# Performance work log

Measured on AMD Instinct MI355X. Metric: run time of the kernel, lower is better.

The kernel has to match this reference:

```python
import jax, jax.numpy as jnp
import numpy as np

# Config mirroring init kwargs (bias_base_type='full', no bos/eos, n_channels=1)
SHAPE_ = 64          # side of the 2D grid; seq_len = SHAPE_**2
N_CHANNELS = 1
N_HEADS = 16
EMB_DIM = 64
BATCH = 8
SEQ_LEN = SHAPE_ * SHAPE_ * N_CHANNELS
N = 2 * SHAPE_ - 1   # linear-convolution length


def setup_inputs() -> dict:
    key = jax.random.key(0)
    k1, k2 = jax.random.split(key)
    v = jax.random.normal(k1, (BATCH, SEQ_LEN, N_HEADS, EMB_DIM), dtype=jnp.float32)
    w = jax.random.normal(k2, (1, N_HEADS, N), dtype=jnp.float32)
    return {"v": v, "w": w}


def reference(v, w):
    shape_ = SHAPE_
    n = 2 * shape_ - 1
    B, S, H, E = v.shape
    C = N_CHANNELS

    # _compute_z_fft with bias_base_type='full', seq_len=shape_:
    # z = w[..., shape_-seq_len : shape_+seq_len-1] == w[..., 0:n]
    z_fft = jnp.fft.rfft(w[..., :n])                       # (1, H, n//2+1)

    # [B,S,H,E] -> [B,E,H,S] -> [B,E,H,s1,s2,C] -> [B,E,C,s1,H,s2]
    v_ = jnp.transpose(v, (0, 3, 2, 1)).reshape(B, E, H, shape_, shape_, C)
    v_ = jnp.transpose(v_, (0, 1, 5, 3, 2, 4))

    pad = ((0, 0),) * 4 + ((shape_ - 1, 0),)
    # sum over s1 (axis -3) -> function of s2; left-pad and rfft
    v_m_fft = jnp.fft.rfft(jnp.pad(v_.sum(-3), pad))       # [B,E,C,H,nr]
    # swap s1/s2, sum over s2 -> function of s1
    u_m_fft = jnp.fft.rfft(jnp.pad(jnp.transpose(v_, (0, 1, 2, 5, 4, 3)).sum(-3), pad))

    zf = jnp.expand_dims(z_fft, axis=1)                    # (1, 1, H, nr) broadcasts
    RxV = jnp.fft.irfft(v_m_fft * zf, n=n)[..., :shape_]   # [B,E,C,H,shape_]
    RxU = jnp.fft.irfft(u_m_fft * zf, n=n)[..., :shape_]   # [B,E,C,H,shape_]

    # outer sum over (s1, s2) grid
    pbv = RxV[..., None, :] + RxU[..., None]               # [B,E,C,H,s1,s2]
    pbv = pbv.reshape(B, E, C, H, shape_ * shape_)
    pbv = jnp.transpose(pbv, (0, 1, 3, 4, 2)).reshape(B, E, H, S)
    return jnp.transpose(pbv, (0, 3, 2, 1))                # [B, S, H, E]
```

## Files before the change

kernel.cpp:

```cpp
#include <hip/hip_runtime.h>


typedef float f4 __attribute__((ext_vector_type(4)));

__global__ __launch_bounds__(256, 4) void k1_reduce(
    const f4* __restrict__ v4,
    f4* __restrict__ vm_part,
    f4* __restrict__ um_ws)
{
    __shared__ f4 um_w[4][16][8];

    const int bid   = blockIdx.x;
    const int hcb   = bid & 31;
    const int slice = (bid >> 5) & 3;
    const int b     = bid >> 7;
    const int t     = threadIdx.x;
    const int slot  = t & 7;
    const int rowth = t >> 3;
    const int wv    = t >> 6;
    const int he4   = hcb * 8 + slot;

    const f4* base = v4 + ((size_t)(b * 4096 + slice * 1024 + rowth) * 256 + he4);

    f4 um_acc[16];
#pragma unroll
    for (int j = 0; j < 16; ++j) um_acc[j] = (f4)0.f;
    f4 vm0 = (f4)0.f, vm1 = (f4)0.f;

#pragma unroll
    for (int s1l = 0; s1l < 16; ++s1l) {
        f4 a  = __builtin_nontemporal_load(base + s1l * 16384);
        f4 b4 = __builtin_nontemporal_load(base + s1l * 16384 + 8192);
        um_acc[s1l] += a + b4;
        vm0 += a;
        vm1 += b4;
    }

    vm_part[((size_t)(slice * 8 + b) * 64 + rowth) * 256 + he4]      = vm0;
    vm_part[((size_t)(slice * 8 + b) * 64 + rowth + 32) * 256 + he4] = vm1;

#pragma unroll
    for (int j = 0; j < 16; ++j) {
        f4 s = um_acc[j];
        s.x += __shfl_xor(s.x, 8);  s.y += __shfl_xor(s.y, 8);
        s.z += __shfl_xor(s.z, 8);  s.w += __shfl_xor(s.w, 8);
        s.x += __shfl_xor(s.x, 16); s.y += __shfl_xor(s.y, 16);
        s.z += __shfl_xor(s.z, 16); s.w += __shfl_xor(s.w, 16);
        s.x += __shfl_xor(s.x, 32); s.y += __shfl_xor(s.y, 32);
        s.z += __shfl_xor(s.z, 32); s.w += __shfl_xor(s.w, 32);
        if ((t & 63) < 8) um_w[wv][j][slot] = s;
    }
    __syncthreads();

    if (t < 128) {
        const int s1l = t >> 3;
        const int sl2 = t & 7;
        f4 s = um_w[0][s1l][sl2] + um_w[1][s1l][sl2]
             + um_w[2][s1l][sl2] + um_w[3][s1l][sl2];
        um_ws[((size_t)b * 64 + slice * 16 + s1l) * 256 + hcb * 8 + sl2] = s;
    }
}

__global__ __launch_bounds__(256) void k2_matvec(
    const f4* __restrict__ vm_part,
    const f4* __restrict__ um_ws,
    const float* __restrict__ w,
    f4* __restrict__ rxv,
    f4* __restrict__ rxu)
{
    __shared__ f4 vm_s[64][16];
    __shared__ f4 um_s[64][16];
    __shared__ float w_s[128];

    const int bid = blockIdx.x;
    const int h   = bid & 15;
    const int b   = bid >> 4;
    const int t   = threadIdx.x;

    if (t < 128) w_s[t] = w[h * 127 + (t == 127 ? 0 : t)];

    {
        const int e4 = t & 15;
        const int sg = t >> 4;
#pragma unroll
        for (int r = 0; r < 4; ++r) {
            const int s2 = sg + 16 * r;
            f4 acc = vm_part[((size_t)(0 * 8 + b) * 64 + s2) * 256 + h * 16 + e4]
                   + vm_part[((size_t)(1 * 8 + b) * 64 + s2) * 256 + h * 16 + e4]
                   + vm_part[((size_t)(2 * 8 + b) * 64 + s2) * 256 + h * 16 + e4]
                   + vm_part[((size_t)(3 * 8 + b) * 64 + s2) * 256 + h * 16 + e4];
            vm_s[s2][e4] = acc;
            um_s[s2][e4] = um_ws[((size_t)b * 64 + s2) * 256 + h * 16 + e4];
        }
    }
    __syncthreads();

    {
        const int e4 = t & 15;
        const int T0 = (t >> 4) * 4;
        f4 aV0 = (f4)0.f, aV1 = (f4)0.f, aV2 = (f4)0.f, aV3 = (f4)0.f;
        f4 aU0 = (f4)0.f, aU1 = (f4)0.f, aU2 = (f4)0.f, aU3 = (f4)0.f;
        float W0 = w_s[T0 + 64], W1 = w_s[T0 + 65];
        float W2v = w_s[T0 + 66], W3v = w_s[T0 + 67];
        for (int k = 0; k < 64; ++k) {
            f4 vmv = vm_s[k][e4];
            f4 umv = um_s[k][e4];
            aV0 += W0 * vmv;  aU0 += W0 * umv;
            aV1 += W1 * vmv;  aU1 += W1 * umv;
            aV2 += W2v * vmv; aU2 += W2v * umv;
            aV3 += W3v * vmv; aU3 += W3v * umv;
            if (k < 63) {
                float nw = w_s[T0 + 63 - k];
                W3v = W2v; W2v = W1; W1 = W0; W0 = nw;
            }
        }
        const size_t o = (size_t)(b * 16 + h) * 64 * 16 + e4;
        rxv[o + (T0 + 0) * 16] = aV0; rxv[o + (T0 + 1) * 16] = aV1;
        rxv[o + (T0 + 2) * 16] = aV2; rxv[o + (T0 + 3) * 16] = aV3;
        rxu[o + (T0 + 0) * 16] = aU0; rxu[o + (T0 + 1) * 16] = aU1;
        rxu[o + (T0 + 2) * 16] = aU2; rxu[o + (T0 + 3) * 16] = aU3;
    }
}

__global__ __launch_bounds__(256) void k3_write(
    const f4* __restrict__ rxv,
    const f4* __restrict__ rxu,
    f4* __restrict__ out4)
{
    const int bid  = blockIdx.x;
    const int t    = threadIdx.x;
    const int sidb = bid * 4;
    const int b    = sidb >> 12;
    const int s1   = (sidb >> 6) & 63;
    const int s2b  = sidb & 63;
    const int h    = t >> 4;
    const int e4   = t & 15;

    const size_t g = (size_t)(b * 16 + h) * 64;
    const f4 ru = rxu[(g + s1) * 16 + e4];
    f4* outp = out4 + ((size_t)(b * 4096 + s1 * 64 + s2b) * 256 + t);

#pragma unroll
    for (int r = 0; r < 4; ++r) {
        f4 rv = rxv[(g + s2b + r) * 16 + e4];
        __builtin_nontemporal_store(ru + rv, outp + r * 256);
    }
}

extern "C" void kernel_launch(void* const* d_in, const int* in_sizes, int n_in,
                              void* d_out, int out_size, void* d_ws, size_t ws_size,
                              hipStream_t stream) {
    const f4*    v4 = (const f4*)d_in[0];
    const float* w  = (const float*)d_in[1];
    f4* out4 = (f4*)d_out;

    f4* ws4     = (f4*)d_ws;
    f4* vm_part = ws4;
    f4* um_ws   = ws4 + 524288;
    f4* rxv     = ws4 + 655360;
    f4* rxu     = ws4 + 786432;

    k1_reduce<<<1024, 256, 0, stream>>>(v4, vm_part, um_ws);
    k2_matvec<<<128, 256, 0, stream>>>(vm_part, um_ws, w, rxv, rxu);
    k3_write<<<8192, 256, 0, stream>>>(rxv, rxu, out4);
}
```

Baseline: 243.8 us.

## Fuse Toeplitz matvec and broadcast output write into one kernel

Merges the matvec and output-write kernels. Each of 1024 blocks recomputes the full RxV vector for its (b,h) plus RxU for its group of 8 s1 rows, then writes those rows straight from shared memory. This removes one kernel launch and the rxv/rxu workspace round trip. In exchange, the RxV matvec and the vm_part reductions are repeated 8 times across blocks, and the write phase now runs on 1024 blocks instead of 8192, each storing more.

```diff
diff --git a/kernel.cpp b/kernel.cpp
--- a/kernel.cpp
+++ b/kernel.cpp
@@ -61,89 +61,77 @@
     }
 }
 
-__global__ __launch_bounds__(256) void k2_matvec(
+__global__ __launch_bounds__(256) void k2_fused(
     const f4* __restrict__ vm_part,
     const f4* __restrict__ um_ws,
     const float* __restrict__ w,
-    f4* __restrict__ rxv,
-    f4* __restrict__ rxu)
+    f4* __restrict__ out4)
 {
     __shared__ f4 vm_s[64][16];
     __shared__ f4 um_s[64][16];
     __shared__ float w_s[128];
 
     const int bid = blockIdx.x;
+    const int s1g = bid >> 7;
+    const int b   = (bid >> 4) & 7;
     const int h   = bid & 15;
-    const int b   = bid >> 4;
     const int t   = threadIdx.x;
+    const int e4  = t & 15;
+    const int tg  = t >> 4;
 
     if (t < 128) w_s[t] = w[h * 127 + (t == 127 ? 0 : t)];
 
-    {
-        const int e4 = t & 15;
-        const int sg = t >> 4;
 #pragma unroll
-        for (int r = 0; r < 4; ++r) {
-            const int s2 = sg + 16 * r;
-            f4 acc = vm_part[((size_t)(0 * 8 + b) * 64 + s2) * 256 + h * 16 + e4]
-                   + vm_part[((size_t)(1 * 8 + b) * 64 + s2) * 256 + h * 16 + e4]
-                   + vm_part[((size_t)(2 * 8 + b) * 64 + s2) * 256 + h * 16 + e4]
-                   + vm_part[((size_t)(3 * 8 + b) * 64 + s2) * 256 + h * 16 + e4];
-            vm_s[s2][e4] = acc;
-            um_s[s2][e4] = um_ws[((size_t)b * 64 + s2) * 256 + h * 16 + e4];
+    for (int r = 0; r < 4; ++r) {
+        const int k = tg + 16 * r;
+        f4 acc = vm_part[((size_t)(0 * 8 + b) * 64 + k) * 256 + h * 16 + e4]
+               + vm_part[((size_t)(1 * 8 + b) * 64 + k) * 256 + h * 16 + e4]
+               + vm_part[((size_t)(2 * 8 + b) * 64 + k) * 256 + h * 16 + e4]
+               + vm_part[((size_t)(3 * 8 + b) * 64 + k) * 256 + h * 16 + e4];
+        vm_s[k][e4] = acc;
+        um_s[k][e4] = um_ws[((size_t)b * 64 + k) * 256 + h * 16 + e4];
+    }
+    __syncthreads();
+
+    const int T0 = tg * 4;
+    const int s1loc = tg & 7;
+    const int s1w = s1g * 8 + s1loc;
+    f4 aV0 = (f4)0.f, aV1 = (f4)0.f, aV2 = (f4)0.f, aV3 = (f4)0.f;
+    f4 aU  = (f4)0.f;
+    float W0 = w_s[T0 + 64], W1 = w_s[T0 + 65];
+    float W2v = w_s[T0 + 66], W3v = w_s[T0 + 67];
+    float WU = w_s[s1w + 64];
+    for (int k = 0; k < 64; ++k) {
+        f4 vmv = vm_s[k][e4];
+        f4 umv = um_s[k][e4];
+        aV0 += W0 * vmv;  aV1 += W1 * vmv;
+        aV2 += W2v * vmv; aV3 += W3v * vmv;
+        aU  += WU * umv;
+        if (k < 63) {
+            float nw = w_s[T0 + 63 - k];
+            W3v = W2v; W2v = W1; W1 = W0; W0 = nw;
+            WU = w_s[s1w + 63 - k];
         }
     }
     __syncthreads();
+    vm_s[T0 + 0][e4] = aV0; vm_s[T0 + 1][e4] = aV1;
+    vm_s[T0 + 2][e4] = aV2; vm_s[T0 + 3][e4] = aV3;
+    if (tg < 8) um_s[tg][e4] = aU;
+    __syncthreads();
 
-    {
-        const int e4 = t & 15;
-        const int T0 = (t >> 4) * 4;
-        f4 aV0 = (f4)0.f, aV1 = (f4)0.f, aV2 = (f4)0.f, aV3 = (f4)0.f;
-        f4 aU0 = (f4)0.f, aU1 = (f4)0.f, aU2 = (f4)0.f, aU3 = (f4)0.f;
-        float W0 = w_s[T0 + 64], W1 = w_s[T0 + 65];
-        float W2v = w_s[T0 + 66], W3v = w_s[T0 + 67];
-        for (int k = 0; k < 64; ++k) {
-            f4 vmv = vm_s[k][e4];
-            f4 umv = um_s[k][e4];
-            aV0 += W0 * vmv;  aU0 += W0 * umv;
-            aV1 += W1 * vmv;  aU1 += W1 * umv;
-            aV2 += W2v * vmv; aU2 += W2v * umv;
-            aV3 += W3v * vmv; aU3 += W3v * umv;
-            if (k < 63) {
-                float nw = w_s[T0 + 63 - k];
-                W3v = W2v; W2v = W1; W1 = W0; W0 = nw;
-            }
-        }
-        const size_t o = (size_t)(b * 16 + h) * 64 * 16 + e4;
-        rxv[o + (T0 + 0) * 16] = aV0; rxv[o + (T0 + 1) * 16] = aV1;
-        rxv[o + (T0 + 2) * 16] = aV2; rxv[o + (T0 + 3) * 16] = aV3;
-        rxu[o + (T0 + 0) * 16] = aU0; rxu[o + (T0 + 1) * 16] = aU1;
-        rxu[o + (T0 + 2) * 16] = aU2; rxu[o + (T0 + 3) * 16] = aU3;
-    }
-}
-
-__global__ __launch_bounds__(256) void k3_write(
-    const f4* __restrict__ rxv,
-    const f4* __restrict__ rxu,
-    f4* __restrict__ out4)
-{
-    const int bid  = blockIdx.x;
-    const int t    = threadIdx.x;
-    const int sidb = bid * 4;
-    const int b    = sidb >> 12;
-    const int s1   = (sidb >> 6) & 63;
-    const int s2b  = sidb & 63;
-    const int h    = t >> 4;
-    const int e4   = t & 15;
-
-    const size_t g = (size_t)(b * 16 + h) * 64;
-    const f4 ru = rxu[(g + s1) * 16 + e4];
-    f4* outp = out4 + ((size_t)(b * 4096 + s1 * 64 + s2b) * 256 + t);
-
+    const f4 rv0 = vm_s[tg +  0][e4];
+    const f4 rv1 = vm_s[tg + 16][e4];
+    const f4 rv2 = vm_s[tg + 32][e4];
+    const f4 rv3 = vm_s[tg + 48][e4];
+    f4* obase = out4 + (size_t)b * 4096 * 256 + (size_t)h * 16 + e4;
 #pragma unroll
-    for (int r = 0; r < 4; ++r) {
-        f4 rv = rxv[(g + s2b + r) * 16 + e4];
-        __builtin_nontemporal_store(ru + rv, outp + r * 256);
+    for (int s1l = 0; s1l < 8; ++s1l) {
+        const f4 ru = um_s[s1l][e4];
+        f4* orow = obase + (size_t)(s1g * 8 + s1l) * 64 * 256;
+        __builtin_nontemporal_store(ru + rv0, orow + (size_t)(tg +  0) * 256);
+        __builtin_nontemporal_store(ru + rv1, orow + (size_t)(tg + 16) * 256);
+        __builtin_nontemporal_store(ru + rv2, orow + (size_t)(tg + 32) * 256);
+        __builtin_nontemporal_store(ru + rv3, orow + (size_t)(tg + 48) * 256);
     }
 }
 
@@ -157,10 +145,7 @@
     f4* ws4     = (f4*)d_ws;
     f4* vm_part = ws4;
     f4* um_ws   = ws4 + 524288;
-    f4* rxv     = ws4 + 655360;
-    f4* rxu     = ws4 + 786432;
 
     k1_reduce<<<1024, 256, 0, stream>>>(v4, vm_part, um_ws);
-    k2_matvec<<<128, 256, 0, stream>>>(vm_part, um_ws, w, rxv, rxu);
-    k3_write<<<8192, 256, 0, stream>>>(rxv, rxu, out4);
+    k2_fused<<<1024, 256, 0, stream>>>(vm_part, um_ws, w, out4);
 }
```

Measured after the change: 245.3 us. No clear change (+0.6%).
